# Optimization experiments

Measured on AMD Instinct MI355X. Metric: run time of the kernel, lower is better.

The kernel has to match this reference:

```python
import jax, jax.numpy as jnp
import numpy as np

# Deterministic hyperparameters (tuples with equal bounds collapse to constants)
MASK_RATIO = 0.6
BLOCK_RATIO = 0.05
ADJUST_RATIO = 0.1  # inverse_block_masking=False -> used with negative sign
MULTI_MASK = 2


def setup_inputs() -> dict:
    key = jax.random.key(0)
    k1, k2, k3 = jax.random.split(key, 3)
    B, P, F = 64, 16384, 3
    centers = jax.random.normal(k1, (B, P, F), dtype=jnp.float32)
    # torch.rand calls inside forward, made explicit inputs for determinism
    rand_centers = jax.random.uniform(k2, (B * MULTI_MASK, P), dtype=jnp.float32)
    rand_mask = jax.random.uniform(k3, (B * MULTI_MASK, P), dtype=jnp.float32)
    return {"centers": centers, "rand_centers": rand_centers, "rand_mask": rand_mask}


def reference(centers, rand_centers, rand_mask):
    B, P, F = centers.shape
    Bm = B * MULTI_MASK
    num_masks = round(MASK_RATIO * P)            # 9830
    block_size = int(BLOCK_RATIO * P)            # 819
    # inverse_block_masking=False: ratio=mask_ratio, adjust=-adjust_ratio
    block_fraction = (MASK_RATIO - ADJUST_RATIO) / block_size
    num_centers = round(P * block_fraction)      # 10

    # random block-center selection via argsort of uniform noise
    center_idx = jnp.argsort(rand_centers, axis=-1)[:, :num_centers]   # [Bm, C]
    cen = jnp.repeat(centers, MULTI_MASK, axis=0)                       # [Bm, P, F]
    sel = jnp.take_along_axis(cen, center_idx[:, :, None], axis=1)      # [Bm, C, F]

    # brute-force KNN: squared euclidean distances [Bm, C, P]
    d2 = (jnp.sum(sel * sel, -1)[:, :, None]
          + jnp.sum(cen * cen, -1)[:, None, :]
          - 2.0 * jnp.einsum('bcf,bpf->bcp', sel, cen))
    knn_idx = jax.lax.top_k(-d2, block_size)[1]                          # [Bm, C, K]

    rows = jnp.arange(Bm)[:, None]
    # scatter False at knn indices, then invert (process_mask = ~x)
    mask = jnp.ones((Bm, P), dtype=bool).at[rows, knn_idx.reshape(Bm, -1)].set(False)
    mask = ~mask  # True = inside a block

    # prioritize block positions, fill remainder randomly up to num_masks
    flip = jnp.where(mask, -rand_mask, rand_mask)
    mask_indices = jnp.argsort(flip, axis=-1)[:, :num_masks]             # [Bm, M]
    final_mask = jnp.zeros((Bm, P), dtype=bool).at[rows, mask_indices].set(True)
    return final_mask
```

## Files before the change

### kernel.cpp

```cpp
#include <hip/hip_runtime.h>


#define PP     16384
#define NROW   128
#define NC     10
#define KNN    819
#define NMASK  9830
#define NT     512
#define PER_T  (PP / NT)
#define CAP2   2048
#define CPT2   (CAP2 / NT)

#define UNI_WORDS_PER_ROW (PP / 32)
#define WS_CL_U32   (NROW * 16)

__device__ __forceinline__ unsigned mapf(float f) {
    unsigned u = __float_as_uint(f);
    return (u & 0x80000000u) ? ~u : (u | 0x80000000u);
}

__device__ __forceinline__ float
d2_core(float cx, float cy, float cz, float sx, float sy, float sz, float s2)
{
    const float q2 = __fadd_rn(__fadd_rn(__fmul_rn(cx, cx), __fmul_rn(cy, cy)),
                               __fmul_rn(cz, cz));
    float dot = __fmul_rn(sx, cx);
    dot = __fmaf_rn(sy, cy, dot);
    dot = __fmaf_rn(sz, cz, dot);
    return __fsub_rn(__fadd_rn(s2, q2), __fmul_rn(2.0f, dot));
}

__device__ void hist_pick(unsigned* hist, volatile unsigned* sh, int nbins,
                          int* kk_io, unsigned* bin_out)
{
    const int t = threadIdx.x, lane = t & 63, wv = t >> 6;
    const int kk = *kk_io;
    int c = 0, x = 0;
    if (t < nbins) {
        c = (int)hist[t]; x = c;
        #pragma unroll
        for (int off = 1; off < 64; off <<= 1) {
            const int y = __shfl_up(x, off, 64);
            if (lane >= off) x += y;
        }
        if (lane == 63) sh[4 + wv] = (unsigned)x;
    }
    __syncthreads();
    if (t < nbins) {
        int base = 0;
        for (int w = 0; w < wv; ++w) base += (int)sh[4 + w];
        x += base;
        const int e = x - c;
        if (e < kk && kk <= x) { sh[0] = (unsigned)t; sh[1] = (unsigned)(kk - e); }
    }
    __syncthreads();
    *bin_out = sh[0];
    *kk_io = (int)sh[1];
    __syncthreads();
}

template <int BPT>
__device__ void pick_bpt(unsigned* hist, volatile unsigned* sh,
                         int* kk_io, unsigned* bin_out)
{
    const int t = threadIdx.x, lane = t & 63, wv = t >> 6;
    const int kk = *kk_io;
    unsigned c[BPT]; int s = 0;
    #pragma unroll
    for (int i = 0; i < BPT; ++i) { c[i] = hist[t * BPT + i]; s += (int)c[i]; }
    int x = s;
    #pragma unroll
    for (int off = 1; off < 64; off <<= 1) {
        const int y = __shfl_up(x, off, 64);
        if (lane >= off) x += y;
    }
    if (lane == 63) sh[4 + wv] = (unsigned)x;
    __syncthreads();
    int base = 0;
    for (int w = 0; w < wv; ++w) base += (int)sh[4 + w];
    x += base;
    const int e = x - s;
    if (e < kk && kk <= x) {
        int cum = e; unsigned bin = 0, rank = 0; bool found = false;
        #pragma unroll
        for (int i = 0; i < BPT; ++i) {
            if (!found && kk <= cum + (int)c[i]) {
                bin = (unsigned)(t * BPT + i); rank = (unsigned)(kk - cum); found = true;
            }
            cum += (int)c[i];
        }
        sh[0] = bin; sh[1] = rank;
    }
    __syncthreads();
    *bin_out = sh[0];
    *kk_io = (int)sh[1];
    __syncthreads();
}

struct Lvl { int shift; int bins; };

template <class FK>
__device__ void narrow_cand(const FK& fullkey, unsigned short* cand, unsigned* ccnt,
                            unsigned* hist, volatile unsigned* sh,
                            unsigned C, int kk, unsigned vpref,
                            const Lvl* lv, int nlv,
                            unsigned& vstar, unsigned& pstar)
{
    const int t = threadIdx.x;
    for (int li = 0; li < nlv && C > 64u; ++li) {
        const int shift = lv[li].shift, bins = lv[li].bins;
        const unsigned mask = (unsigned)(bins - 1);
        for (int i = t; i < bins; i += NT) hist[i] = 0;
        __syncthreads();
        unsigned ci[CPT2], bb[CPT2]; bool va[CPT2];
        #pragma unroll
        for (int i = 0; i < CPT2; ++i) {
            const unsigned pos = (unsigned)(i * NT + t);
            va[i] = pos < C;
            ci[i] = va[i] ? (unsigned)cand[pos] : 0u;
            bb[i] = 0u;
            if (va[i]) { bb[i] = (fullkey(ci[i]) >> shift) & mask; atomicAdd(&hist[bb[i]], 1u); }
        }
        __syncthreads();
        unsigned bl;
        if (bins == 1024) pick_bpt<2>(hist, sh, &kk, &bl);
        else              hist_pick(hist, sh, bins, &kk, &bl);
        vpref |= bl << shift;
        if (t == 0) *ccnt = 0;
        __syncthreads();
        #pragma unroll
        for (int i = 0; i < CPT2; ++i)
            if (va[i] && bb[i] == bl) cand[atomicAdd(ccnt, 1u)] = (unsigned short)ci[i];
        __syncthreads();
        C = *ccnt;
        __syncthreads();
    }
    if (C <= 64u) {
        if (t < 64) {
            unsigned v = 0xFFFFFFFFu, pidx = 0xFFFFu;
            if ((unsigned)t < C) { pidx = (unsigned)cand[t]; v = fullkey(pidx); }
            int rank = 0;
            for (unsigned j = 0; j < C; ++j) {
                const unsigned vj = __shfl(v, (int)j, 64);
                const unsigned pj = __shfl(pidx, (int)j, 64);
                if (vj < v || (vj == v && pj < pidx)) ++rank;
            }
            if ((unsigned)t < C && rank == kk - 1) { sh[0] = v; sh[1] = pidx; }
        }
        __syncthreads();
        vstar = sh[0]; pstar = sh[1];
        __syncthreads();
        return;
    }
    vstar = vpref;
    if (t < 128) hist[t] = 0;
    __syncthreads();
    {
        unsigned ci[CPT2], bb[CPT2]; bool va[CPT2];
        #pragma unroll
        for (int i = 0; i < CPT2; ++i) {
            const unsigned pos = (unsigned)(i * NT + t);
            va[i] = pos < C;
            ci[i] = va[i] ? (unsigned)cand[pos] : 0u;
            bb[i] = ci[i] >> 7;
            if (va[i]) atomicAdd(&hist[bb[i]], 1u);
        }
        __syncthreads();
        unsigned bl; hist_pick(hist, sh, 128, &kk, &bl);
        if (t == 0) *ccnt = 0;
        __syncthreads();
        #pragma unroll
        for (int i = 0; i < CPT2; ++i)
            if (va[i] && bb[i] == bl) cand[atomicAdd(ccnt, 1u)] = (unsigned short)ci[i];
        __syncthreads();
        C = *ccnt;
        __syncthreads();
    }
    if (t < 64) {
        unsigned p0 = 0xFFFFFFFFu, p1 = 0xFFFFFFFFu;
        if ((unsigned)t < C)        p0 = (unsigned)cand[t];
        if ((unsigned)(t + 64) < C) p1 = (unsigned)cand[t + 64];
        int r0 = 0, r1 = 0;
        for (unsigned j = 0; j < C; ++j) {
            const unsigned pj = (j < 64) ? __shfl(p0, (int)j, 64)
                                         : __shfl(p1, (int)(j - 64), 64);
            if (pj < p0) ++r0;
            if (pj < p1) ++r1;
        }
        if ((unsigned)t < C && r0 == kk - 1)        sh[1] = p0;
        if ((unsigned)(t + 64) < C && r1 == kk - 1) sh[1] = p1;
    }
    __syncthreads();
    pstar = sh[1];
    __syncthreads();
}

template <class FK>
__device__ void fallback_radix(const FK& fullkey, unsigned* hist, volatile unsigned* sh,
                               int k, unsigned& vstar, unsigned& pstar)
{
    const int t = threadIdx.x;
    int kk = k; unsigned prefix = 0;
    for (int pass = 0; pass < 4; ++pass) {
        const int shift = 24 - pass * 8;
        if (t < 256) hist[t] = 0;
        __syncthreads();
        for (int j = 0; j < PER_T; ++j) {
            const unsigned p = (unsigned)(j * NT + t);
            const unsigned v = fullkey(p);
            bool in = (pass == 0) || ((v >> (shift + 8)) == prefix);
            if (in) atomicAdd(&hist[(v >> shift) & 255u], 1u);
        }
        __syncthreads();
        unsigned b; hist_pick(hist, sh, 256, &kk, &b);
        prefix = (prefix << 8) | b;
    }
    vstar = prefix;
    unsigned ipref = 0;
    for (int pass = 0; pass < 2; ++pass) {
        const int shift = 7 - pass * 7;
        if (t < 128) hist[t] = 0;
        __syncthreads();
        for (int j = 0; j < PER_T; ++j) {
            const unsigned p = (unsigned)(j * NT + t);
            bool in = (fullkey(p) == vstar);
            if (in && pass != 0) in = ((p >> (shift + 7)) == ipref);
            if (in) atomicAdd(&hist[(p >> shift) & 127u], 1u);
        }
        __syncthreads();
        unsigned b; hist_pick(hist, sh, 128, &kk, &b);
        ipref = (ipref << 7) | b;
    }
    pstar = ipref;
}

template <class FK>
__device__ void select16(const FK& fullkey, const unsigned short* keys16,
                         unsigned* hist, volatile unsigned* sh,
                         unsigned short* cand, unsigned* ccnt, int k,
                         unsigned& vstar, unsigned& pstar)
{
    const int t = threadIdx.x;
    int kk = k;
    unsigned b0; pick_bpt<8>(hist, sh, &kk, &b0);

    if (t == 0) *ccnt = 0;
    __syncthreads();
    #pragma unroll 4
    for (int j = 0; j < PER_T; ++j) {
        const unsigned p = (unsigned)(j * NT + t);
        if ((unsigned)(keys16[p] >> 4) == b0) {
            const unsigned pos = atomicAdd(ccnt, 1u);
            if (pos < CAP2) cand[pos] = (unsigned short)p;
        }
    }
    __syncthreads();
    unsigned C = *ccnt;
    __syncthreads();
    if (C <= CAP2) {
        const Lvl lvA[2] = { {10, 1024}, {0, 1024} };
        narrow_cand(fullkey, cand, ccnt, hist, sh, C, kk, b0 << 20, lvA, 2, vstar, pstar);
        return;
    }
    if (t < 16) hist[t] = 0;
    __syncthreads();
    #pragma unroll 4
    for (int j = 0; j < PER_T; ++j) {
        const unsigned p = (unsigned)(j * NT + t);
        const unsigned k16 = keys16[p];
        if ((k16 >> 4) == b0) atomicAdd(&hist[k16 & 15u], 1u);
    }
    __syncthreads();
    unsigned b1; hist_pick(hist, sh, 16, &kk, &b1);
    const unsigned pref16 = (b0 << 4) | b1;
    if (t == 0) *ccnt = 0;
    __syncthreads();
    #pragma unroll 4
    for (int j = 0; j < PER_T; ++j) {
        const unsigned p = (unsigned)(j * NT + t);
        if ((unsigned)keys16[p] == pref16) {
            const unsigned pos = atomicAdd(ccnt, 1u);
            if (pos < CAP2) cand[pos] = (unsigned short)p;
        }
    }
    __syncthreads();
    C = *ccnt;
    __syncthreads();
    if (C <= CAP2) {
        const Lvl lvB[2] = { {8, 256}, {0, 256} };
        narrow_cand(fullkey, cand, ccnt, hist, sh, C, kk, pref16 << 16, lvB, 2, vstar, pstar);
        return;
    }
    fallback_radix(fullkey, hist, sh, k, vstar, pstar);
}

#define DECL_SHARED                                         \
    __shared__ unsigned short keys16[PP];                   \
    __shared__ unsigned hist[4096];                         \
    __shared__ unsigned sh_[8];                             \
    __shared__ unsigned ccnt_s;                             \
    __shared__ unsigned short cand[CAP2];                   \
    volatile unsigned* sh = (volatile unsigned*)sh_;

extern "C" __global__ void __launch_bounds__(NT, 6)
bpm_centers(const float* __restrict__ rand_centers, unsigned* __restrict__ ws_cl,
            unsigned* __restrict__ uni)
{
    DECL_SHARED
    __shared__ unsigned clist[16];
    __shared__ unsigned pcnt;

    const int bm = blockIdx.x;
    const int t  = threadIdx.x;
    uni[bm * NT + t] = 0u;

    const float* rcrow = rand_centers + (size_t)bm * PP;
    auto fullkey = [rcrow](unsigned p) -> unsigned { return mapf(rcrow[p]); };

    #pragma unroll
    for (int i = 0; i < 8; ++i) hist[t * 8 + i] = 0;
    if (t == 0) pcnt = 0;
    __syncthreads();
    #pragma unroll 4
    for (int j = 0; j < PER_T; ++j) {
        const int p = j * NT + t;
        const unsigned k32 = fullkey((unsigned)p);
        keys16[p] = (unsigned short)(k32 >> 16);
        atomicAdd(&hist[k32 >> 20], 1u);
    }
    __syncthreads();

    unsigned vs, ps;
    select16(fullkey, keys16, hist, sh, cand, &ccnt_s, NC, vs, ps);
    const unsigned vs16 = vs >> 16;

    #pragma unroll 4
    for (int j = 0; j < PER_T; ++j) {
        const unsigned p = (unsigned)(j * NT + t);
        const unsigned k16 = keys16[p];
        bool sel = false;
        if (k16 < vs16) sel = true;
        else if (k16 == vs16) {
            const unsigned v = fullkey(p);
            sel = (v < vs) || (v == vs && p <= ps);
        }
        if (sel) clist[atomicAdd(&pcnt, 1u)] = p;
    }
    __syncthreads();
    if (t < NC) ws_cl[bm * 16 + t] = clist[t];
}

extern "C" __global__ void __launch_bounds__(NT, 6)
bpm_knn(const float* __restrict__ centers, const unsigned* __restrict__ ws_cl,
        unsigned* __restrict__ uni)
{
    DECL_SHARED
    const int c  = blockIdx.x;
    const int bm = blockIdx.y;
    const int b  = bm >> 1;
    const int t  = threadIdx.x;
    const float* crow = centers + (size_t)b * PP * 3;

    const int ci = (int)ws_cl[bm * 16 + c];
    const float sx = crow[ci * 3 + 0];
    const float sy = crow[ci * 3 + 1];
    const float sz = crow[ci * 3 + 2];
    const float s2 = __fadd_rn(__fadd_rn(__fmul_rn(sx, sx), __fmul_rn(sy, sy)),
                               __fmul_rn(sz, sz));
    auto fullkey = [crow, sx, sy, sz, s2](unsigned p) -> unsigned {
        const float cx = crow[3 * p + 0], cy = crow[3 * p + 1], cz = crow[3 * p + 2];
        return mapf(d2_core(cx, cy, cz, sx, sy, sz, s2));
    };

    #pragma unroll
    for (int i = 0; i < 8; ++i) hist[t * 8 + i] = 0;
    __syncthreads();
    #pragma unroll 4
    for (int j = 0; j < PER_T; ++j) {
        const int p = j * NT + t;
        const unsigned k32 = fullkey((unsigned)p);
        keys16[p] = (unsigned short)(k32 >> 16);
        atomicAdd(&hist[k32 >> 20], 1u);
    }
    __syncthreads();

    unsigned vs, ps;
    select16(fullkey, keys16, hist, sh, cand, &ccnt_s, KNN, vs, ps);
    const unsigned vs16 = vs >> 16;

    unsigned* urow = uni + (size_t)bm * UNI_WORDS_PER_ROW;
    #pragma unroll 4
    for (int j = 0; j < PER_T; ++j) {
        const unsigned p = (unsigned)(j * NT + t);
        const unsigned k16 = keys16[p];
        bool sel = false;
        if (k16 < vs16) sel = true;
        else if (k16 == vs16) {
            const unsigned v = fullkey(p);
            sel = (v < vs) || (v == vs && p <= ps);
        }
        const unsigned long long bmask = __ballot(sel);
        if ((t & 63) == 0 && bmask) {
            const int wbase = (int)(p >> 5);
            const unsigned lo = (unsigned)bmask;
            const unsigned hi = (unsigned)(bmask >> 32);
            if (lo) atomicOr(&urow[wbase], lo);
            if (hi) atomicOr(&urow[wbase + 1], hi);
        }
    }
}

extern "C" __global__ void __launch_bounds__(NT, 6)
bpm_final(const float* __restrict__ rand_mask, const unsigned* __restrict__ uni,
          int* __restrict__ out)
{
    DECL_SHARED
    const int bm = blockIdx.x;
    const int t  = threadIdx.x;
    const float* rmrow = rand_mask + (size_t)bm * PP;
    const unsigned* urow = uni + (size_t)bm * UNI_WORDS_PER_ROW;

    auto fullkey = [rmrow, urow](unsigned p) -> unsigned {
        const float r = rmrow[p];
        const bool inb = (urow[p >> 5] >> (p & 31)) & 1u;
        return mapf(inb ? -r : r);
    };

    #pragma unroll
    for (int i = 0; i < 8; ++i) hist[t * 8 + i] = 0;
    __syncthreads();
    #pragma unroll 4
    for (int j = 0; j < PER_T; ++j) {
        const int p = j * NT + t;
        const unsigned k32 = fullkey((unsigned)p);
        keys16[p] = (unsigned short)(k32 >> 16);
        atomicAdd(&hist[k32 >> 20], 1u);
    }
    __syncthreads();

    unsigned vs, ps;
    select16(fullkey, keys16, hist, sh, cand, &ccnt_s, NMASK, vs, ps);
    const unsigned vs16 = vs >> 16;

    int* orow = out + (size_t)bm * PP;
    #pragma unroll 4
    for (int j = 0; j < PER_T; ++j) {
        const unsigned p = (unsigned)(j * NT + t);
        const unsigned k16 = keys16[p];
        bool sel = false;
        if (k16 < vs16) sel = true;
        else if (k16 == vs16) {
            const unsigned v = fullkey(p);
            sel = (v < vs) || (v == vs && p <= ps);
        }
        orow[p] = sel ? 1 : 0;
    }
}

extern "C" void kernel_launch(void* const* d_in, const int* in_sizes, int n_in,
                              void* d_out, int out_size, void* d_ws, size_t ws_size,
                              hipStream_t stream)
{
    (void)in_sizes; (void)n_in; (void)out_size; (void)ws_size;
    const float* centers      = (const float*)d_in[0];
    const float* rand_centers = (const float*)d_in[1];
    const float* rand_mask    = (const float*)d_in[2];
    int* out = (int*)d_out;

    unsigned* ws_cl = (unsigned*)d_ws;
    unsigned* uni   = ws_cl + WS_CL_U32;

    bpm_centers<<<dim3(NROW), dim3(NT), 0, stream>>>(rand_centers, ws_cl, uni);
    bpm_knn<<<dim3(NC, NROW), dim3(NT), 0, stream>>>(centers, ws_cl, uni);
    bpm_final<<<dim3(NROW), dim3(NT), 0, stream>>>(rand_mask, uni, out);
}
```

Before: 179.3 us.

## Double block size, vectorize key-building loads, and remap KNN grid for L2 reuse

Raises the thread count per block from 512 to 1024 and rewrites the first histogram and key pass of all three kernels to use float4 loads, handling four points per thread per iteration. The KNN kernel loads three float4 per four points instead of scalar xyz loads. It also flattens the KNN grid so that the ten center blocks of eight consecutive rows are grouped together, which is meant to improve L2 reuse of the centers data. The risks are the larger blocks, which can mean more barrier cost and fewer resident blocks per CU, and the histogram-pick paths that now rely on different per-thread bin counts.

```diff
diff --git a/kernel.cpp b/kernel.cpp
--- a/kernel.cpp
+++ b/kernel.cpp
@@ -6,13 +6,14 @@
 #define NC     10
 #define KNN    819
 #define NMASK  9830
-#define NT     512
+#define NT     1024
 #define PER_T  (PP / NT)
+#define KG_IT  (PP / (NT * 4))
 #define CAP2   2048
 #define CPT2   (CAP2 / NT)
 
-#define UNI_WORDS_PER_ROW (PP / 32)
-#define WS_CL_U32   (NROW * 16)
+#define UNI_WPR   512
+#define WS_CL_U32 (NROW * 16)
 
 __device__ __forceinline__ unsigned mapf(float f) {
     unsigned u = __float_as_uint(f);
@@ -110,7 +111,7 @@
     for (int li = 0; li < nlv && C > 64u; ++li) {
         const int shift = lv[li].shift, bins = lv[li].bins;
         const unsigned mask = (unsigned)(bins - 1);
-        for (int i = t; i < bins; i += NT) hist[i] = 0;
+        if (t < bins) hist[t] = 0;
         __syncthreads();
         unsigned ci[CPT2], bb[CPT2]; bool va[CPT2];
         #pragma unroll
@@ -123,8 +124,7 @@
         }
         __syncthreads();
         unsigned bl;
-        if (bins == 1024) pick_bpt<2>(hist, sh, &kk, &bl);
-        else              hist_pick(hist, sh, bins, &kk, &bl);
+        hist_pick(hist, sh, bins, &kk, &bl);
         vpref |= bl << shift;
         if (t == 0) *ccnt = 0;
         __syncthreads();
@@ -242,7 +242,7 @@
 {
     const int t = threadIdx.x;
     int kk = k;
-    unsigned b0; pick_bpt<8>(hist, sh, &kk, &b0);
+    unsigned b0; pick_bpt<4>(hist, sh, &kk, &b0);
 
     if (t == 0) *ccnt = 0;
     __syncthreads();
@@ -297,12 +297,12 @@
 #define DECL_SHARED                                         \
     __shared__ unsigned short keys16[PP];                   \
     __shared__ unsigned hist[4096];                         \
-    __shared__ unsigned sh_[8];                             \
+    __shared__ unsigned sh_[24];                            \
     __shared__ unsigned ccnt_s;                             \
     __shared__ unsigned short cand[CAP2];                   \
     volatile unsigned* sh = (volatile unsigned*)sh_;
 
-extern "C" __global__ void __launch_bounds__(NT, 6)
+extern "C" __global__ void __launch_bounds__(NT, 8)
 bpm_centers(const float* __restrict__ rand_centers, unsigned* __restrict__ ws_cl,
             unsigned* __restrict__ uni)
 {
@@ -312,21 +312,28 @@
 
     const int bm = blockIdx.x;
     const int t  = threadIdx.x;
-    uni[bm * NT + t] = 0u;
+    if (t < UNI_WPR) uni[bm * UNI_WPR + t] = 0u;
 
     const float* rcrow = rand_centers + (size_t)bm * PP;
     auto fullkey = [rcrow](unsigned p) -> unsigned { return mapf(rcrow[p]); };
 
     #pragma unroll
-    for (int i = 0; i < 8; ++i) hist[t * 8 + i] = 0;
+    for (int i = 0; i < 4; ++i) hist[t * 4 + i] = 0;
     if (t == 0) pcnt = 0;
     __syncthreads();
-    #pragma unroll 4
-    for (int j = 0; j < PER_T; ++j) {
-        const int p = j * NT + t;
-        const unsigned k32 = fullkey((unsigned)p);
-        keys16[p] = (unsigned short)(k32 >> 16);
-        atomicAdd(&hist[k32 >> 20], 1u);
+    #pragma unroll
+    for (int j = 0; j < KG_IT; ++j) {
+        const int q = j * (NT * 4) + t * 4;
+        const float4 v = *(const float4*)(rcrow + q);
+        const unsigned k0 = mapf(v.x), k1 = mapf(v.y), k2 = mapf(v.z), k3 = mapf(v.w);
+        *(ushort4*)(keys16 + q) = make_ushort4((unsigned short)(k0 >> 16),
+                                               (unsigned short)(k1 >> 16),
+                                               (unsigned short)(k2 >> 16),
+                                               (unsigned short)(k3 >> 16));
+        atomicAdd(&hist[k0 >> 20], 1u);
+        atomicAdd(&hist[k1 >> 20], 1u);
+        atomicAdd(&hist[k2 >> 20], 1u);
+        atomicAdd(&hist[k3 >> 20], 1u);
     }
     __syncthreads();
 
@@ -350,15 +357,17 @@
     if (t < NC) ws_cl[bm * 16 + t] = clist[t];
 }
 
-extern "C" __global__ void __launch_bounds__(NT, 6)
+extern "C" __global__ void __launch_bounds__(NT, 8)
 bpm_knn(const float* __restrict__ centers, const unsigned* __restrict__ ws_cl,
         unsigned* __restrict__ uni)
 {
     DECL_SHARED
-    const int c  = blockIdx.x;
-    const int bm = blockIdx.y;
-    const int b  = bm >> 1;
-    const int t  = threadIdx.x;
+    const int bid   = blockIdx.x;
+    const int inner = bid >> 3;
+    const int bm    = (inner / NC) * 8 + (bid & 7);
+    const int c     = inner % NC;
+    const int b     = bm >> 1;
+    const int t     = threadIdx.x;
     const float* crow = centers + (size_t)b * PP * 3;
 
     const int ci = (int)ws_cl[bm * 16 + c];
@@ -373,14 +382,25 @@
     };
 
     #pragma unroll
-    for (int i = 0; i < 8; ++i) hist[t * 8 + i] = 0;
-    __syncthreads();
-    #pragma unroll 4
-    for (int j = 0; j < PER_T; ++j) {
-        const int p = j * NT + t;
-        const unsigned k32 = fullkey((unsigned)p);
-        keys16[p] = (unsigned short)(k32 >> 16);
-        atomicAdd(&hist[k32 >> 20], 1u);
+    for (int i = 0; i < 4; ++i) hist[t * 4 + i] = 0;
+    __syncthreads();
+    #pragma unroll
+    for (int j = 0; j < KG_IT; ++j) {
+        const int q = j * (NT * 4) + t * 4;
+        const float4* cp4 = (const float4*)(crow + 3 * q);
+        const float4 A = cp4[0], Bv = cp4[1], Cv = cp4[2];
+        const unsigned k0 = mapf(d2_core(A.x,  A.y,  A.z,  sx, sy, sz, s2));
+        const unsigned k1 = mapf(d2_core(A.w,  Bv.x, Bv.y, sx, sy, sz, s2));
+        const unsigned k2 = mapf(d2_core(Bv.z, Bv.w, Cv.x, sx, sy, sz, s2));
+        const unsigned k3 = mapf(d2_core(Cv.y, Cv.z, Cv.w, sx, sy, sz, s2));
+        *(ushort4*)(keys16 + q) = make_ushort4((unsigned short)(k0 >> 16),
+                                               (unsigned short)(k1 >> 16),
+                                               (unsigned short)(k2 >> 16),
+                                               (unsigned short)(k3 >> 16));
+        atomicAdd(&hist[k0 >> 20], 1u);
+        atomicAdd(&hist[k1 >> 20], 1u);
+        atomicAdd(&hist[k2 >> 20], 1u);
+        atomicAdd(&hist[k3 >> 20], 1u);
     }
     __syncthreads();
 
@@ -388,7 +408,7 @@
     select16(fullkey, keys16, hist, sh, cand, &ccnt_s, KNN, vs, ps);
     const unsigned vs16 = vs >> 16;
 
-    unsigned* urow = uni + (size_t)bm * UNI_WORDS_PER_ROW;
+    unsigned* urow = uni + (size_t)bm * UNI_WPR;
     #pragma unroll 4
     for (int j = 0; j < PER_T; ++j) {
         const unsigned p = (unsigned)(j * NT + t);
@@ -410,7 +430,7 @@
     }
 }
 
-extern "C" __global__ void __launch_bounds__(NT, 6)
+extern "C" __global__ void __launch_bounds__(NT, 8)
 bpm_final(const float* __restrict__ rand_mask, const unsigned* __restrict__ uni,
           int* __restrict__ out)
 {
@@ -418,7 +438,7 @@
     const int bm = blockIdx.x;
     const int t  = threadIdx.x;
     const float* rmrow = rand_mask + (size_t)bm * PP;
-    const unsigned* urow = uni + (size_t)bm * UNI_WORDS_PER_ROW;
+    const unsigned* urow = uni + (size_t)bm * UNI_WPR;
 
     auto fullkey = [rmrow, urow](unsigned p) -> unsigned {
         const float r = rmrow[p];
@@ -427,14 +447,25 @@
     };
 
     #pragma unroll
-    for (int i = 0; i < 8; ++i) hist[t * 8 + i] = 0;
-    __syncthreads();
-    #pragma unroll 4
-    for (int j = 0; j < PER_T; ++j) {
-        const int p = j * NT + t;
-        const unsigned k32 = fullkey((unsigned)p);
-        keys16[p] = (unsigned short)(k32 >> 16);
-        atomicAdd(&hist[k32 >> 20], 1u);
+    for (int i = 0; i < 4; ++i) hist[t * 4 + i] = 0;
+    __syncthreads();
+    #pragma unroll
+    for (int j = 0; j < KG_IT; ++j) {
+        const int q = j * (NT * 4) + t * 4;
+        const float4 v = *(const float4*)(rmrow + q);
+        const unsigned w = urow[q >> 5];
+        const unsigned k0 = mapf(((w >> ((q + 0) & 31)) & 1u) ? -v.x : v.x);
+        const unsigned k1 = mapf(((w >> ((q + 1) & 31)) & 1u) ? -v.y : v.y);
+        const unsigned k2 = mapf(((w >> ((q + 2) & 31)) & 1u) ? -v.z : v.z);
+        const unsigned k3 = mapf(((w >> ((q + 3) & 31)) & 1u) ? -v.w : v.w);
+        *(ushort4*)(keys16 + q) = make_ushort4((unsigned short)(k0 >> 16),
+                                               (unsigned short)(k1 >> 16),
+                                               (unsigned short)(k2 >> 16),
+                                               (unsigned short)(k3 >> 16));
+        atomicAdd(&hist[k0 >> 20], 1u);
+        atomicAdd(&hist[k1 >> 20], 1u);
+        atomicAdd(&hist[k2 >> 20], 1u);
+        atomicAdd(&hist[k3 >> 20], 1u);
     }
     __syncthreads();
 
@@ -471,6 +502,6 @@
     unsigned* uni   = ws_cl + WS_CL_U32;
 
     bpm_centers<<<dim3(NROW), dim3(NT), 0, stream>>>(rand_centers, ws_cl, uni);
-    bpm_knn<<<dim3(NC, NROW), dim3(NT), 0, stream>>>(centers, ws_cl, uni);
+    bpm_knn<<<dim3(NROW * NC), dim3(NT), 0, stream>>>(centers, ws_cl, uni);
     bpm_final<<<dim3(NROW), dim3(NT), 0, stream>>>(rand_mask, uni, out);
 }
```

Result: faster. 157.4 us (-12.2%).

## Keep 16-bit keys in registers, cache candidate keys, and widen row kernels

Applied to the files above, without the earlier changes.

Moves the per-element 16-bit key cache from a 32 KB shared array into packed registers. This cuts shared memory per block so more blocks fit per CU. Candidate collection now stores the full 32-bit key next to the position, so the narrowing passes no longer recompute keys (including the KNN distance or a gather from global memory). The single-row kernels go to 1024 threads, the KNN grid is flattened so neighbouring blocks share rows, and the second-level 16-bin refinement is dropped, so oversized candidate sets go straight to the full radix fallback. The trade-off is higher register pressure and a more expensive slow path when a bin overflows.

```diff
diff --git a/kernel.cpp b/kernel.cpp
--- a/kernel.cpp
+++ b/kernel.cpp
@@ -6,13 +6,10 @@
 #define NC     10
 #define KNN    819
 #define NMASK  9830
-#define NT     512
-#define PER_T  (PP / NT)
-#define CAP2   2048
-#define CPT2   (CAP2 / NT)
-
-#define UNI_WORDS_PER_ROW (PP / 32)
-#define WS_CL_U32   (NROW * 16)
+#define HB     4096
+#define CAP    2048
+#define UNI_WPR   512
+#define WS_CL_U32 (NROW * 16)
 
 __device__ __forceinline__ unsigned mapf(float f) {
     unsigned u = __float_as_uint(f);
@@ -30,8 +27,8 @@
     return __fsub_rn(__fadd_rn(s2, q2), __fmul_rn(2.0f, dot));
 }
 
-__device__ void hist_pick(unsigned* hist, volatile unsigned* sh, int nbins,
-                          int* kk_io, unsigned* bin_out)
+__device__ __forceinline__ void hist_pick(unsigned* hist, unsigned* sh, int nbins,
+                                          int* kk_io, unsigned* bin_out)
 {
     const int t = threadIdx.x, lane = t & 63, wv = t >> 6;
     const int kk = *kk_io;
@@ -59,9 +56,9 @@
     __syncthreads();
 }
 
-template <int BPT>
-__device__ void pick_bpt(unsigned* hist, volatile unsigned* sh,
-                         int* kk_io, unsigned* bin_out)
+template <int BPT, int NTT>
+__device__ __forceinline__ void pick_bpt(unsigned* hist, unsigned* sh,
+                                         int* kk_io, unsigned* bin_out)
 {
     const int t = threadIdx.x, lane = t & 63, wv = t >> 6;
     const int kk = *kk_io;
@@ -97,40 +94,44 @@
     __syncthreads();
 }
 
-struct Lvl { int shift; int bins; };
-
-template <class FK>
-__device__ void narrow_cand(const FK& fullkey, unsigned short* cand, unsigned* ccnt,
-                            unsigned* hist, volatile unsigned* sh,
-                            unsigned C, int kk, unsigned vpref,
-                            const Lvl* lv, int nlv,
-                            unsigned& vstar, unsigned& pstar)
-{
+template <int NTT>
+__device__ __forceinline__ void
+narrow_cand(unsigned* cand_v, unsigned short* cand_p,
+            unsigned* ccnt, unsigned* hist, unsigned* sh,
+            unsigned C, int kk, unsigned vpref,
+            unsigned& vstar, unsigned& pstar)
+{
+    constexpr int CPT = CAP / NTT;
     const int t = threadIdx.x;
-    for (int li = 0; li < nlv && C > 64u; ++li) {
-        const int shift = lv[li].shift, bins = lv[li].bins;
-        const unsigned mask = (unsigned)(bins - 1);
-        for (int i = t; i < bins; i += NT) hist[i] = 0;
-        __syncthreads();
-        unsigned ci[CPT2], bb[CPT2]; bool va[CPT2];
-        #pragma unroll
-        for (int i = 0; i < CPT2; ++i) {
-            const unsigned pos = (unsigned)(i * NT + t);
+    #pragma unroll
+    for (int li = 0; li < 2; ++li) {
+        if (C <= 64u) break;
+        const int shift = (li == 0) ? 10 : 0;
+        for (int i = t; i < 1024; i += NTT) hist[i] = 0;
+        __syncthreads();
+        unsigned vv[CPT], pi_[CPT], bb[CPT]; bool va[CPT];
+        #pragma unroll
+        for (int i = 0; i < CPT; ++i) {
+            const unsigned pos = (unsigned)(i * NTT + t);
             va[i] = pos < C;
-            ci[i] = va[i] ? (unsigned)cand[pos] : 0u;
-            bb[i] = 0u;
-            if (va[i]) { bb[i] = (fullkey(ci[i]) >> shift) & mask; atomicAdd(&hist[bb[i]], 1u); }
+            vv[i] = va[i] ? cand_v[pos] : 0u;
+            pi_[i] = va[i] ? (unsigned)cand_p[pos] : 0u;
+            bb[i] = (vv[i] >> shift) & 1023u;
+            if (va[i]) atomicAdd(&hist[bb[i]], 1u);
         }
         __syncthreads();
         unsigned bl;
-        if (bins == 1024) pick_bpt<2>(hist, sh, &kk, &bl);
-        else              hist_pick(hist, sh, bins, &kk, &bl);
+        if constexpr (NTT >= 1024) hist_pick(hist, sh, 1024, &kk, &bl);
+        else                       pick_bpt<1024 / NTT, NTT>(hist, sh, &kk, &bl);
         vpref |= bl << shift;
         if (t == 0) *ccnt = 0;
         __syncthreads();
         #pragma unroll
-        for (int i = 0; i < CPT2; ++i)
-            if (va[i] && bb[i] == bl) cand[atomicAdd(ccnt, 1u)] = (unsigned short)ci[i];
+        for (int i = 0; i < CPT; ++i)
+            if (va[i] && bb[i] == bl) {
+                const unsigned pos = atomicAdd(ccnt, 1u);
+                cand_v[pos] = vv[i]; cand_p[pos] = (unsigned short)pi_[i];
+            }
         __syncthreads();
         C = *ccnt;
         __syncthreads();
@@ -138,7 +139,7 @@
     if (C <= 64u) {
         if (t < 64) {
             unsigned v = 0xFFFFFFFFu, pidx = 0xFFFFu;
-            if ((unsigned)t < C) { pidx = (unsigned)cand[t]; v = fullkey(pidx); }
+            if ((unsigned)t < C) { v = cand_v[t]; pidx = (unsigned)cand_p[t]; }
             int rank = 0;
             for (unsigned j = 0; j < C; ++j) {
                 const unsigned vj = __shfl(v, (int)j, 64);
@@ -156,13 +157,13 @@
     if (t < 128) hist[t] = 0;
     __syncthreads();
     {
-        unsigned ci[CPT2], bb[CPT2]; bool va[CPT2];
-        #pragma unroll
-        for (int i = 0; i < CPT2; ++i) {
-            const unsigned pos = (unsigned)(i * NT + t);
+        unsigned pi_[CPT], bb[CPT]; bool va[CPT];
+        #pragma unroll
+        for (int i = 0; i < CPT; ++i) {
+            const unsigned pos = (unsigned)(i * NTT + t);
             va[i] = pos < C;
-            ci[i] = va[i] ? (unsigned)cand[pos] : 0u;
-            bb[i] = ci[i] >> 7;
+            pi_[i] = va[i] ? (unsigned)cand_p[pos] : 0u;
+            bb[i] = pi_[i] >> 7;
             if (va[i]) atomicAdd(&hist[bb[i]], 1u);
         }
         __syncthreads();
@@ -170,16 +171,17 @@
         if (t == 0) *ccnt = 0;
         __syncthreads();
         #pragma unroll
-        for (int i = 0; i < CPT2; ++i)
-            if (va[i] && bb[i] == bl) cand[atomicAdd(ccnt, 1u)] = (unsigned short)ci[i];
+        for (int i = 0; i < CPT; ++i)
+            if (va[i] && bb[i] == bl)
+                cand_p[atomicAdd(ccnt, 1u)] = (unsigned short)pi_[i];
         __syncthreads();
         C = *ccnt;
         __syncthreads();
     }
     if (t < 64) {
         unsigned p0 = 0xFFFFFFFFu, p1 = 0xFFFFFFFFu;
-        if ((unsigned)t < C)        p0 = (unsigned)cand[t];
-        if ((unsigned)(t + 64) < C) p1 = (unsigned)cand[t + 64];
+        if ((unsigned)t < C)        p0 = (unsigned)cand_p[t];
+        if ((unsigned)(t + 64) < C) p1 = (unsigned)cand_p[t + 64];
         int r0 = 0, r1 = 0;
         for (unsigned j = 0; j < C; ++j) {
             const unsigned pj = (j < 64) ? __shfl(p0, (int)j, 64)
@@ -195,18 +197,20 @@
     __syncthreads();
 }
 
-template <class FK>
-__device__ void fallback_radix(const FK& fullkey, unsigned* hist, volatile unsigned* sh,
-                               int k, unsigned& vstar, unsigned& pstar)
-{
+template <int NTT, class FK>
+__device__ __forceinline__ void
+fallback_radix(const FK& fullkey, unsigned* hist, unsigned* sh, int k,
+               unsigned& vstar, unsigned& pstar)
+{
+    constexpr int PT = PP / NTT;
     const int t = threadIdx.x;
     int kk = k; unsigned prefix = 0;
     for (int pass = 0; pass < 4; ++pass) {
         const int shift = 24 - pass * 8;
         if (t < 256) hist[t] = 0;
         __syncthreads();
-        for (int j = 0; j < PER_T; ++j) {
-            const unsigned p = (unsigned)(j * NT + t);
+        for (int j = 0; j < PT; ++j) {
+            const unsigned p = (unsigned)(j * NTT + t);
             const unsigned v = fullkey(p);
             bool in = (pass == 0) || ((v >> (shift + 8)) == prefix);
             if (in) atomicAdd(&hist[(v >> shift) & 255u], 1u);
@@ -221,8 +225,8 @@
         const int shift = 7 - pass * 7;
         if (t < 128) hist[t] = 0;
         __syncthreads();
-        for (int j = 0; j < PER_T; ++j) {
-            const unsigned p = (unsigned)(j * NT + t);
+        for (int j = 0; j < PT; ++j) {
+            const unsigned p = (unsigned)(j * NTT + t);
             bool in = (fullkey(p) == vstar);
             if (in && pass != 0) in = ((p >> (shift + 7)) == ipref);
             if (in) atomicAdd(&hist[(p >> shift) & 127u], 1u);
@@ -234,113 +238,72 @@
     pstar = ipref;
 }
 
-template <class FK>
-__device__ void select16(const FK& fullkey, const unsigned short* keys16,
-                         unsigned* hist, volatile unsigned* sh,
-                         unsigned short* cand, unsigned* ccnt, int k,
-                         unsigned& vstar, unsigned& pstar)
-{
-    const int t = threadIdx.x;
-    int kk = k;
-    unsigned b0; pick_bpt<8>(hist, sh, &kk, &b0);
-
-    if (t == 0) *ccnt = 0;
-    __syncthreads();
-    #pragma unroll 4
-    for (int j = 0; j < PER_T; ++j) {
-        const unsigned p = (unsigned)(j * NT + t);
-        if ((unsigned)(keys16[p] >> 4) == b0) {
-            const unsigned pos = atomicAdd(ccnt, 1u);
-            if (pos < CAP2) cand[pos] = (unsigned short)p;
-        }
-    }
-    __syncthreads();
-    unsigned C = *ccnt;
-    __syncthreads();
-    if (C <= CAP2) {
-        const Lvl lvA[2] = { {10, 1024}, {0, 1024} };
-        narrow_cand(fullkey, cand, ccnt, hist, sh, C, kk, b0 << 20, lvA, 2, vstar, pstar);
-        return;
-    }
-    if (t < 16) hist[t] = 0;
-    __syncthreads();
-    #pragma unroll 4
-    for (int j = 0; j < PER_T; ++j) {
-        const unsigned p = (unsigned)(j * NT + t);
-        const unsigned k16 = keys16[p];
-        if ((k16 >> 4) == b0) atomicAdd(&hist[k16 & 15u], 1u);
-    }
-    __syncthreads();
-    unsigned b1; hist_pick(hist, sh, 16, &kk, &b1);
-    const unsigned pref16 = (b0 << 4) | b1;
-    if (t == 0) *ccnt = 0;
-    __syncthreads();
-    #pragma unroll 4
-    for (int j = 0; j < PER_T; ++j) {
-        const unsigned p = (unsigned)(j * NT + t);
-        if ((unsigned)keys16[p] == pref16) {
-            const unsigned pos = atomicAdd(ccnt, 1u);
-            if (pos < CAP2) cand[pos] = (unsigned short)p;
-        }
-    }
-    __syncthreads();
-    C = *ccnt;
-    __syncthreads();
-    if (C <= CAP2) {
-        const Lvl lvB[2] = { {8, 256}, {0, 256} };
-        narrow_cand(fullkey, cand, ccnt, hist, sh, C, kk, pref16 << 16, lvB, 2, vstar, pstar);
-        return;
-    }
-    fallback_radix(fullkey, hist, sh, k, vstar, pstar);
-}
-
-#define DECL_SHARED                                         \
-    __shared__ unsigned short keys16[PP];                   \
-    __shared__ unsigned hist[4096];                         \
-    __shared__ unsigned sh_[8];                             \
-    __shared__ unsigned ccnt_s;                             \
-    __shared__ unsigned short cand[CAP2];                   \
-    volatile unsigned* sh = (volatile unsigned*)sh_;
-
-extern "C" __global__ void __launch_bounds__(NT, 6)
+#define KR_SET(kr, j, k16) do { \
+    if ((j) & 1) kr[(j) >> 1] |= (k16) << 16; else kr[(j) >> 1] = (k16); } while (0)
+#define KR_GET(kr, j) (((kr)[(j) >> 1] >> (((j) & 1) * 16)) & 0xFFFFu)
+
+#define NTC 1024
+#define PTC (PP / NTC)
+
+extern "C" __global__ void __launch_bounds__(NTC, 4)
 bpm_centers(const float* __restrict__ rand_centers, unsigned* __restrict__ ws_cl,
             unsigned* __restrict__ uni)
 {
-    DECL_SHARED
+    __shared__ unsigned hist[HB];
+    __shared__ unsigned cand_v[CAP];
+    __shared__ unsigned short cand_p[CAP];
+    __shared__ unsigned sh[24];
+    __shared__ unsigned ccnt;
     __shared__ unsigned clist[16];
     __shared__ unsigned pcnt;
 
     const int bm = blockIdx.x;
     const int t  = threadIdx.x;
-    uni[bm * NT + t] = 0u;
+    if (t < UNI_WPR) uni[bm * UNI_WPR + t] = 0u;
 
     const float* rcrow = rand_centers + (size_t)bm * PP;
     auto fullkey = [rcrow](unsigned p) -> unsigned { return mapf(rcrow[p]); };
 
-    #pragma unroll
-    for (int i = 0; i < 8; ++i) hist[t * 8 + i] = 0;
-    if (t == 0) pcnt = 0;
-    __syncthreads();
-    #pragma unroll 4
-    for (int j = 0; j < PER_T; ++j) {
-        const int p = j * NT + t;
-        const unsigned k32 = fullkey((unsigned)p);
-        keys16[p] = (unsigned short)(k32 >> 16);
+    unsigned kr[PTC / 2];
+    #pragma unroll
+    for (int i = 0; i < HB / NTC; ++i) hist[t * (HB / NTC) + i] = 0;
+    if (t == 0) { ccnt = 0; pcnt = 0; }
+    __syncthreads();
+    #pragma unroll
+    for (int j = 0; j < PTC; ++j) {
+        const unsigned p = (unsigned)(j * NTC + t);
+        const unsigned k32 = fullkey(p);
+        KR_SET(kr, j, k32 >> 16);
         atomicAdd(&hist[k32 >> 20], 1u);
     }
     __syncthreads();
 
+    int kk = NC;
+    unsigned b0; pick_bpt<HB / NTC, NTC>(hist, sh, &kk, &b0);
+    #pragma unroll
+    for (int j = 0; j < PTC; ++j) {
+        const unsigned k16 = KR_GET(kr, j);
+        if ((k16 >> 4) == b0) {
+            const unsigned p = (unsigned)(j * NTC + t);
+            const unsigned k32 = fullkey(p);
+            const unsigned pos = atomicAdd(&ccnt, 1u);
+            if (pos < CAP) { cand_v[pos] = k32; cand_p[pos] = (unsigned short)p; }
+        }
+    }
+    __syncthreads();
+    unsigned C = ccnt;
+    __syncthreads();
     unsigned vs, ps;
-    select16(fullkey, keys16, hist, sh, cand, &ccnt_s, NC, vs, ps);
+    if (C <= CAP) narrow_cand<NTC>(cand_v, cand_p, &ccnt, hist, sh, C, kk, b0 << 20, vs, ps);
+    else          fallback_radix<NTC>(fullkey, hist, sh, NC, vs, ps);
     const unsigned vs16 = vs >> 16;
 
-    #pragma unroll 4
-    for (int j = 0; j < PER_T; ++j) {
-        const unsigned p = (unsigned)(j * NT + t);
-        const unsigned k16 = keys16[p];
-        bool sel = false;
-        if (k16 < vs16) sel = true;
-        else if (k16 == vs16) {
+    #pragma unroll
+    for (int j = 0; j < PTC; ++j) {
+        const unsigned p = (unsigned)(j * NTC + t);
+        const unsigned k16 = KR_GET(kr, j);
+        bool sel = k16 < vs16;
+        if (k16 == vs16) {
             const unsigned v = fullkey(p);
             sel = (v < vs) || (v == vs && p <= ps);
         }
@@ -350,15 +313,25 @@
     if (t < NC) ws_cl[bm * 16 + t] = clist[t];
 }
 
-extern "C" __global__ void __launch_bounds__(NT, 6)
+#define NTK 512
+#define PTK (PP / NTK)
+
+extern "C" __global__ void __launch_bounds__(NTK, 8)
 bpm_knn(const float* __restrict__ centers, const unsigned* __restrict__ ws_cl,
         unsigned* __restrict__ uni)
 {
-    DECL_SHARED
-    const int c  = blockIdx.x;
-    const int bm = blockIdx.y;
-    const int b  = bm >> 1;
-    const int t  = threadIdx.x;
+    __shared__ unsigned hist[HB];
+    __shared__ unsigned cand_v[CAP];
+    __shared__ unsigned short cand_p[CAP];
+    __shared__ unsigned sh[24];
+    __shared__ unsigned ccnt;
+
+    const int bid   = blockIdx.x;
+    const int inner = bid >> 3;
+    const int bm    = (inner / NC) * 8 + (bid & 7);
+    const int c     = inner % NC;
+    const int b     = bm >> 1;
+    const int t     = threadIdx.x;
     const float* crow = centers + (size_t)b * PP * 3;
 
     const int ci = (int)ws_cl[bm * 16 + c];
@@ -372,30 +345,47 @@
         return mapf(d2_core(cx, cy, cz, sx, sy, sz, s2));
     };
 
-    #pragma unroll
-    for (int i = 0; i < 8; ++i) hist[t * 8 + i] = 0;
-    __syncthreads();
-    #pragma unroll 4
-    for (int j = 0; j < PER_T; ++j) {
-        const int p = j * NT + t;
-        const unsigned k32 = fullkey((unsigned)p);
-        keys16[p] = (unsigned short)(k32 >> 16);
+    unsigned kr[PTK / 2];
+    #pragma unroll
+    for (int i = 0; i < HB / NTK; ++i) hist[t * (HB / NTK) + i] = 0;
+    if (t == 0) ccnt = 0;
+    __syncthreads();
+    #pragma unroll
+    for (int j = 0; j < PTK; ++j) {
+        const unsigned p = (unsigned)(j * NTK + t);
+        const unsigned k32 = fullkey(p);
+        KR_SET(kr, j, k32 >> 16);
         atomicAdd(&hist[k32 >> 20], 1u);
     }
     __syncthreads();
 
+    int kk = KNN;
+    unsigned b0; pick_bpt<HB / NTK, NTK>(hist, sh, &kk, &b0);
+    #pragma unroll
+    for (int j = 0; j < PTK; ++j) {
+        const unsigned k16 = KR_GET(kr, j);
+        if ((k16 >> 4) == b0) {
+            const unsigned p = (unsigned)(j * NTK + t);
+            const unsigned k32 = fullkey(p);
+            const unsigned pos = atomicAdd(&ccnt, 1u);
+            if (pos < CAP) { cand_v[pos] = k32; cand_p[pos] = (unsigned short)p; }
+        }
+    }
+    __syncthreads();
+    unsigned C = ccnt;
+    __syncthreads();
     unsigned vs, ps;
-    select16(fullkey, keys16, hist, sh, cand, &ccnt_s, KNN, vs, ps);
+    if (C <= CAP) narrow_cand<NTK>(cand_v, cand_p, &ccnt, hist, sh, C, kk, b0 << 20, vs, ps);
+    else          fallback_radix<NTK>(fullkey, hist, sh, KNN, vs, ps);
     const unsigned vs16 = vs >> 16;
 
-    unsigned* urow = uni + (size_t)bm * UNI_WORDS_PER_ROW;
-    #pragma unroll 4
-    for (int j = 0; j < PER_T; ++j) {
-        const unsigned p = (unsigned)(j * NT + t);
-        const unsigned k16 = keys16[p];
-        bool sel = false;
-        if (k16 < vs16) sel = true;
-        else if (k16 == vs16) {
+    unsigned* urow = uni + (size_t)bm * UNI_WPR;
+    #pragma unroll
+    for (int j = 0; j < PTK; ++j) {
+        const unsigned p = (unsigned)(j * NTK + t);
+        const unsigned k16 = KR_GET(kr, j);
+        bool sel = k16 < vs16;
+        if (k16 == vs16) {
             const unsigned v = fullkey(p);
             sel = (v < vs) || (v == vs && p <= ps);
         }
@@ -410,15 +400,20 @@
     }
 }
 
-extern "C" __global__ void __launch_bounds__(NT, 6)
+extern "C" __global__ void __launch_bounds__(NTC, 4)
 bpm_final(const float* __restrict__ rand_mask, const unsigned* __restrict__ uni,
           int* __restrict__ out)
 {
-    DECL_SHARED
+    __shared__ unsigned hist[HB];
+    __shared__ unsigned cand_v[CAP];
+    __shared__ unsigned short cand_p[CAP];
+    __shared__ unsigned sh[24];
+    __shared__ unsigned ccnt;
+
     const int bm = blockIdx.x;
     const int t  = threadIdx.x;
     const float* rmrow = rand_mask + (size_t)bm * PP;
-    const unsigned* urow = uni + (size_t)bm * UNI_WORDS_PER_ROW;
+    const unsigned* urow = uni + (size_t)bm * UNI_WPR;
 
     auto fullkey = [rmrow, urow](unsigned p) -> unsigned {
         const float r = rmrow[p];
@@ -426,30 +421,47 @@
         return mapf(inb ? -r : r);
     };
 
-    #pragma unroll
-    for (int i = 0; i < 8; ++i) hist[t * 8 + i] = 0;
-    __syncthreads();
-    #pragma unroll 4
-    for (int j = 0; j < PER_T; ++j) {
-        const int p = j * NT + t;
-        const unsigned k32 = fullkey((unsigned)p);
-        keys16[p] = (unsigned short)(k32 >> 16);
+    unsigned kr[PTC / 2];
+    #pragma unroll
+    for (int i = 0; i < HB / NTC; ++i) hist[t * (HB / NTC) + i] = 0;
+    if (t == 0) ccnt = 0;
+    __syncthreads();
+    #pragma unroll
+    for (int j = 0; j < PTC; ++j) {
+        const unsigned p = (unsigned)(j * NTC + t);
+        const unsigned k32 = fullkey(p);
+        KR_SET(kr, j, k32 >> 16);
         atomicAdd(&hist[k32 >> 20], 1u);
     }
     __syncthreads();
 
+    int kk = NMASK;
+    unsigned b0; pick_bpt<HB / NTC, NTC>(hist, sh, &kk, &b0);
+    #pragma unroll
+    for (int j = 0; j < PTC; ++j) {
+        const unsigned k16 = KR_GET(kr, j);
+        if ((k16 >> 4) == b0) {
+            const unsigned p = (unsigned)(j * NTC + t);
+            const unsigned k32 = fullkey(p);
+            const unsigned pos = atomicAdd(&ccnt, 1u);
+            if (pos < CAP) { cand_v[pos] = k32; cand_p[pos] = (unsigned short)p; }
+        }
+    }
+    __syncthreads();
+    unsigned C = ccnt;
+    __syncthreads();
     unsigned vs, ps;
-    select16(fullkey, keys16, hist, sh, cand, &ccnt_s, NMASK, vs, ps);
+    if (C <= CAP) narrow_cand<NTC>(cand_v, cand_p, &ccnt, hist, sh, C, kk, b0 << 20, vs, ps);
+    else          fallback_radix<NTC>(fullkey, hist, sh, NMASK, vs, ps);
     const unsigned vs16 = vs >> 16;
 
     int* orow = out + (size_t)bm * PP;
-    #pragma unroll 4
-    for (int j = 0; j < PER_T; ++j) {
-        const unsigned p = (unsigned)(j * NT + t);
-        const unsigned k16 = keys16[p];
-        bool sel = false;
-        if (k16 < vs16) sel = true;
-        else if (k16 == vs16) {
+    #pragma unroll
+    for (int j = 0; j < PTC; ++j) {
+        const unsigned p = (unsigned)(j * NTC + t);
+        const unsigned k16 = KR_GET(kr, j);
+        bool sel = k16 < vs16;
+        if (k16 == vs16) {
             const unsigned v = fullkey(p);
             sel = (v < vs) || (v == vs && p <= ps);
         }
@@ -470,7 +482,7 @@
     unsigned* ws_cl = (unsigned*)d_ws;
     unsigned* uni   = ws_cl + WS_CL_U32;
 
-    bpm_centers<<<dim3(NROW), dim3(NT), 0, stream>>>(rand_centers, ws_cl, uni);
-    bpm_knn<<<dim3(NC, NROW), dim3(NT), 0, stream>>>(centers, ws_cl, uni);
-    bpm_final<<<dim3(NROW), dim3(NT), 0, stream>>>(rand_mask, uni, out);
-}
+    bpm_centers<<<dim3(NROW), dim3(NTC), 0, stream>>>(rand_centers, ws_cl, uni);
+    bpm_knn<<<dim3(NROW * NC), dim3(NTK), 0, stream>>>(centers, ws_cl, uni);
+    bpm_final<<<dim3(NROW), dim3(NTC), 0, stream>>>(rand_mask, uni, out);
+}
```

New measurement: 356.1 us. 1.99x slower.
